# Performance work log

Hardware: AMD Instinct MI355X
Metric: run time of the kernel (lower is better)

Reference implementation:

```python
import jax, jax.numpy as jnp
import numpy as np

EPS = 1e-7          # keras K.epsilon()
MIN_TEMP = 0.1
ALPHA = 0.99999
START_TEMP = 10.0
BATCH, D, BINS, K_OUT = 4096, 20000, 10, 64


def setup_inputs() -> dict:
    key = jax.random.key(0)
    k1, k2, k3 = jax.random.split(key, 3)
    X = jax.random.normal(k1, (BATCH, D), dtype=jnp.float32)
    u = jax.random.normal(k2, (D, BINS), dtype=jnp.float32)
    # keras 'uniform' initializer: U(-0.05, 0.05)
    tinyW = jax.random.uniform(k3, (BINS, K_OUT), dtype=jnp.float32, minval=-0.05, maxval=0.05)
    temp = jnp.float32(START_TEMP)
    return {"X": X, "u": u, "tinyW": tinyW, "temp": temp}


def greedy_assign(p):
    """Greedy bipartite argmax-and-mask assignment (the host loop in the original).
    p: (k, d) scores. Returns (k, d) 0/1 assignment with one 1 per row, unique cols."""
    k, d = p.shape

    def step(pm, _):
        ind = jnp.argmax(pm)            # global argmax over flattened (k, d)
        x = ind // d
        y = ind % d
        pm = pm.at[x, :].set(-1.0).at[:, y].set(-1.0)
        return pm, (x, y)

    _, (xs, ys) = jax.lax.scan(step, p, None, length=k)
    return jnp.zeros((k, d), p.dtype).at[xs, ys].set(1.0)


def reference(X, u, tinyW, temp):
    # al = softmax(u @ tinyW) over output_dim axis, then transpose -> (k, d)
    al = jax.nn.softmax(u @ tinyW, axis=-1).T                  # (k, d)
    logits = jnp.log(10.0 * jnp.clip(al, EPS, 0.9999999))      # (k, d)
    # Gumbel noise: -log(-log(U)), U ~ Uniform(eps, 1)
    nkey = jax.random.key(42)
    uniform = jax.random.uniform(nkey, logits.shape, logits.dtype, EPS, 1.0)
    gumbel = -jnp.log(-jnp.log(uniform))
    # annealed temperature update (K.update in original)
    new_temp = jnp.maximum(jnp.float32(MIN_TEMP), temp * jnp.float32(ALPHA))
    samples = jax.nn.softmax((logits + gumbel) / new_temp, axis=-1)  # (k, d)
    # inference-path discrete selection via greedy argmax-and-mask loop
    discrete = greedy_assign(samples)                           # (k, d)
    # training path: Y = X @ samples^T  (main memory-bound skinny GEMM)
    Y = X @ samples.T                                           # (batch, k)
    return Y, discrete, new_temp
```

## Files before the change

kernel.cpp:

```cpp
#include <hip/hip_runtime.h>
#include <stdint.h>
#include <math.h>

typedef unsigned long long ull;
typedef __attribute__((ext_vector_type(8))) short short8;
typedef __attribute__((ext_vector_type(4))) float f32x4;

#define DD 20000
#define NK 64
#define NB 4096
#define YN (NB * NK)
#define TOTN (YN + NK * DD + 1)
#define KS 16

#define E_OFF   0u
#define RSP_OFF 10240000u
#define CV_OFF  10400256u
#define CC_OFF  10416640u
#define EB_OFF  10433024u
#define IRS_OFF 12993024u
#define P_OFF   12993280u

__device__ __forceinline__ uint32_t tf_bits(uint32_t j) {
  const uint32_t k0 = 0u, k1 = 42u;
  const uint32_t k2 = 0x1BD11BDAu ^ k0 ^ k1;
  uint32_t x0 = k0;
  uint32_t x1 = j + k1;
#define TFR(r) { x0 += x1; x1 = (x1 << r) | (x1 >> (32 - r)); x1 ^= x0; }
  TFR(13) TFR(15) TFR(26) TFR(6)
  x0 += k1; x1 += k2 + 1u;
  TFR(17) TFR(29) TFR(16) TFR(24)
  x0 += k2; x1 += k0 + 2u;
  TFR(13) TFR(15) TFR(26) TFR(6)
  x0 += k0; x1 += k1 + 3u;
  TFR(17) TFR(29) TFR(16) TFR(24)
  x0 += k1; x1 += k2 + 4u;
  TFR(13) TFR(15) TFR(26) TFR(6)
  x0 += k2; x1 += k0 + 5u;
#undef TFR
  return x0 ^ x1;
}

__global__ __launch_bounds__(256) void k_z(
    const float* __restrict__ uu, const float* __restrict__ tw,
    const float* __restrict__ temp, double* __restrict__ E,
    ushort* __restrict__ EB, double* __restrict__ RSP,
    float* __restrict__ disc) {
  __shared__ double tile[NK][65];
  __shared__ double psumw[4][NK];
  const int tid = threadIdx.x;
  const int lane = tid & 63;
  const int wv = tid >> 6;
  const int d0 = blockIdx.x * 64;
  const float nt = fmaxf(0.1f, temp[0] * 0.99999f);
  float w[10];
#pragma unroll
  for (int i = 0; i < 10; ++i) w[i] = tw[i * NK + lane];
  double psum = 0.0;
  for (int it = 0; it < 16; ++it) {
    const int dl = wv * 16 + it;
    const int d = d0 + dl;
    double e = 0.0;
    if (d < DD) {
      float m = 0.f;
#pragma unroll
      for (int i = 0; i < 10; ++i) m = fmaf(uu[d * 10 + i], w[i], m);
      float mx = m;
#pragma unroll
      for (int off = 32; off; off >>= 1) mx = fmaxf(mx, __shfl_xor(mx, off, 64));
      double ee = exp((double)(m - mx));
      double ssum = ee;
#pragma unroll
      for (int off = 32; off; off >>= 1) ssum += __shfl_xor(ssum, off, 64);
      float al = (float)(ee / ssum);
      float c = fminf(fmaxf(al, 1e-7f), 0.9999999f);
      float lg = (float)log((double)(10.0f * c));
      const uint32_t bits = tf_bits((uint32_t)(lane * DD + d));
      float uf = __uint_as_float((bits >> 9) | 0x3f800000u) - 1.0f;
      float uv = fmaxf(1e-7f, uf * (1.0f - 1e-7f) + 1e-7f);
      float g = (float)(-log(-log((double)uv)));
      float z = (lg + g) / nt;
      e = exp((double)z);
    }
    tile[lane][dl] = e;
    psum += e;
  }
  psumw[wv][lane] = psum;
  __syncthreads();
  for (int r0 = 0; r0 < NK; r0 += 4) {
    const int r = r0 + wv;
    const int d = d0 + lane;
    if (d < DD) {
      const double ev = tile[r][lane];
      E[(size_t)r * DD + d] = ev;
      const float ef = (float)ev;
      uint32_t ub = __float_as_uint(ef);
      EB[(size_t)r * DD + d] = (ushort)((ub + 0x7FFFu + ((ub >> 16) & 1u)) >> 16);
    }
  }
  if (wv == 0) {
    double s = psumw[0][lane] + psumw[1][lane] + psumw[2][lane] + psumw[3][lane];
    RSP[(size_t)blockIdx.x * NK + lane] = s;
  }
  const int cg = tid & 15;
  const int r0 = tid >> 4;
  if (d0 + cg * 4 < DD) {
    for (int r = r0; r < NK; r += 16)
      *(float4*)(disc + (size_t)r * DD + d0 + cg * 4) = make_float4(0.f, 0.f, 0.f, 0.f);
  }
}

__global__ __launch_bounds__(256) void k_gr(
    const float* __restrict__ X, const ushort* __restrict__ EB,
    float* __restrict__ P,
    const double* __restrict__ E, const double* __restrict__ RSP,
    float* __restrict__ cv, int* __restrict__ cc, float* __restrict__ invRS) {
  const int tid = threadIdx.x;
  if (blockIdx.x < 64) {
    const int k = blockIdx.x;
    __shared__ double redd[256];
    __shared__ ull keys[2048];
    __shared__ ull wbest[4];
    const double* er = E + (size_t)k * DD;
    double psum = 0.0;
    for (int b = tid; b < 313; b += 256) psum += RSP[(size_t)b * NK + k];
    redd[tid] = psum;
    __syncthreads();
    for (int s = 128; s; s >>= 1) {
      if (tid < s) redd[tid] += redd[tid + s];
      __syncthreads();
    }
    const double sumall = redd[0];
    if (tid == 0) invRS[k] = (float)(1.0 / sumall);
    float tv[8]; int tc[8];
#pragma unroll
    for (int s = 0; s < 8; ++s) { tv[s] = -1.f; tc[s] = 0; }
    for (int d = tid; d < DD; d += 256) {
      float svv = (float)(er[d] / sumall);
      if (svv > tv[7]) {
        float cvr = svv; int ccr = d;
#pragma unroll
        for (int s = 0; s < 8; ++s) {
          bool sw = cvr > tv[s];
          float nv = sw ? cvr : tv[s]; int nc = sw ? ccr : tc[s];
          cvr = sw ? tv[s] : cvr; ccr = sw ? tc[s] : ccr;
          tv[s] = nv; tc[s] = nc;
        }
      }
    }
#pragma unroll
    for (int s = 0; s < 8; ++s)
      keys[(tid << 3) + s] = (((ull)__float_as_uint(tv[s])) << 32)
                           | ((ull)(uint32_t)(32767 - tc[s]) << 11)
                           | ((ull)tid << 3) | (ull)s;
    __syncthreads();
    for (int t = 0; t < NK; ++t) {
      ull best = 0;
#pragma unroll
      for (int s = 0; s < 8; ++s) { ull kk = keys[(tid << 3) + s]; if (kk > best) best = kk; }
#pragma unroll
      for (int off = 32; off; off >>= 1) { ull o = __shfl_xor(best, off, 64); if (o > best) best = o; }
      if ((tid & 63) == 0) wbest[tid >> 6] = best;
      __syncthreads();
      ull win = wbest[0];
#pragma unroll
      for (int wI = 1; wI < 4; ++wI) if (wbest[wI] > win) win = wbest[wI];
      const uint32_t lo = (uint32_t)win;
      const int slot = lo & 7;
      const int owner = (lo >> 3) & 255;
      const int col = 32767 - (int)(lo >> 11);
      if (tid == 0) {
        cv[(k << 6) + t] = __uint_as_float((uint32_t)(win >> 32));
        cc[(k << 6) + t] = col;
      }
      if (tid == owner) keys[(owner << 3) + slot] = 0;
      __syncthreads();
    }
    return;
  }
  const int bx2 = blockIdx.x - 64;
  const int ksp = bx2 >> 6;
  const int by = bx2 & 63;
  const int lane = tid & 63;
  const int wv = tid >> 6;
  const int m16 = lane & 15;
  const int kq = lane >> 4;
  const int mRow = by * 64 + wv * 16 + m16;
  const float* xq = X + (size_t)mRow * DD + ksp * 32 + kq * 8;
  const ushort* bq = EB + (size_t)m16 * DD + ksp * 32 + kq * 8;
  f32x4 acc[4] = {{0,0,0,0},{0,0,0,0},{0,0,0,0},{0,0,0,0}};
  const int jN = (625 - ksp + KS - 1) / KS;

#define LOADBUF(xa, xb, bn, j) { \
    const int o_ = (j) * (KS * 32); \
    xa = *(const float4*)(xq + o_); \
    xb = *(const float4*)(xq + o_ + 4); \
    bn##0 = *(const uint4*)(bq + o_); \
    bn##1 = *(const uint4*)(bq + 16 * DD + o_); \
    bn##2 = *(const uint4*)(bq + 32 * DD + o_); \
    bn##3 = *(const uint4*)(bq + 48 * DD + o_); }

#define COMPUTEBUF(xa, xb, bn) { \
    uint32_t t0=__float_as_uint(xa.x), t1=__float_as_uint(xa.y), t2=__float_as_uint(xa.z), t3=__float_as_uint(xa.w); \
    uint32_t t4=__float_as_uint(xb.x), t5=__float_as_uint(xb.y), t6=__float_as_uint(xb.z), t7=__float_as_uint(xb.w); \
    t0=(t0+0x7FFFu+((t0>>16)&1u))>>16; t1=(t1+0x7FFFu+((t1>>16)&1u))>>16; \
    t2=(t2+0x7FFFu+((t2>>16)&1u))>>16; t3=(t3+0x7FFFu+((t3>>16)&1u))>>16; \
    t4=(t4+0x7FFFu+((t4>>16)&1u))>>16; t5=(t5+0x7FFFu+((t5>>16)&1u))>>16; \
    t6=(t6+0x7FFFu+((t6>>16)&1u))>>16; t7=(t7+0x7FFFu+((t7>>16)&1u))>>16; \
    union { uint32_t u[4]; short8 v; } A_; \
    A_.u[0]=t0|(t1<<16); A_.u[1]=t2|(t3<<16); A_.u[2]=t4|(t5<<16); A_.u[3]=t6|(t7<<16); \
    union { uint4 q; short8 v; } Q0_, Q1_, Q2_, Q3_; \
    Q0_.q = bn##0; Q1_.q = bn##1; Q2_.q = bn##2; Q3_.q = bn##3; \
    acc[0] = __builtin_amdgcn_mfma_f32_16x16x32_bf16(A_.v, Q0_.v, acc[0], 0, 0, 0); \
    acc[1] = __builtin_amdgcn_mfma_f32_16x16x32_bf16(A_.v, Q1_.v, acc[1], 0, 0, 0); \
    acc[2] = __builtin_amdgcn_mfma_f32_16x16x32_bf16(A_.v, Q2_.v, acc[2], 0, 0, 0); \
    acc[3] = __builtin_amdgcn_mfma_f32_16x16x32_bf16(A_.v, Q3_.v, acc[3], 0, 0, 0); }

  float4 xaA, xbA, xaB, xbB, xaC, xbC;
  uint4 bA0, bA1, bA2, bA3, bB0, bB1, bB2, bB3, bC0, bC1, bC2, bC3;
  LOADBUF(xaA, xbA, bA, 0);
  LOADBUF(xaB, xbB, bB, 1);
  LOADBUF(xaC, xbC, bC, 2);
  int j = 0;
  for (; j + 3 < jN; j += 3) {
    COMPUTEBUF(xaA, xbA, bA);
    LOADBUF(xaA, xbA, bA, j + 3);
    COMPUTEBUF(xaB, xbB, bB);
    if (j + 4 < jN) { LOADBUF(xaB, xbB, bB, j + 4); }
    COMPUTEBUF(xaC, xbC, bC);
    if (j + 5 < jN) { LOADBUF(xaC, xbC, bC, j + 5); }
  }
  COMPUTEBUF(xaA, xbA, bA);
  if (j + 1 < jN) { COMPUTEBUF(xaB, xbB, bB); }
  if (j + 2 < jN) { COMPUTEBUF(xaC, xbC, bC); }
#undef LOADBUF
#undef COMPUTEBUF

  float* pp = P + (size_t)ksp * YN;
  const int rBase = by * 64 + wv * 16 + kq * 4;
#pragma unroll
  for (int nt = 0; nt < 4; ++nt)
#pragma unroll
    for (int r = 0; r < 4; ++r)
      pp[(size_t)(rBase + r) * 64 + nt * 16 + m16] = acc[nt][r];
}

__global__ __launch_bounds__(256) void k_tail(
    const float* __restrict__ cv, const int* __restrict__ cc,
    const float* __restrict__ temp, const float* __restrict__ P,
    const float* __restrict__ invRS, float* __restrict__ out) {
  const int tid = threadIdx.x;
  if (blockIdx.x == 0) {
    __shared__ float vf[NK * NK];
    __shared__ int cf[NK * NK];
    __shared__ alignas(16) unsigned char used[DD];
    for (int i = tid; i < 1250; i += 256) ((int4*)used)[i] = make_int4(0, 0, 0, 0);
    for (int i = tid; i < 1024; i += 256) {
      ((float4*)vf)[i] = ((const float4*)cv)[i];
      ((int4*)cf)[i] = ((const int4*)cc)[i];
    }
    __syncthreads();
    if (tid >= 64) return;
    const int lane = tid;
    int ptr = 0;
    float hv = vf[lane << 6];
    int hc = cf[lane << 6];
    bool done = false;
    for (int t = 0; t < NK; ++t) {
      const float v = done ? -1.f : hv;
      float m = v;
#pragma unroll
      for (int off = 32; off; off >>= 1) m = fmaxf(m, __shfl_xor(m, off, 64));
      const ull mask = __ballot(v == m);
      const int row = __ffsll(mask) - 1;
      const int col = __shfl(hc, row, 64);
      if (lane == row) done = true;
      if (lane == 0) {
        used[col] = 1;
        out[YN + (size_t)row * DD + col] = 1.0f;
      }
      asm volatile("s_waitcnt lgkmcnt(0)" ::: "memory");
      if (!done && hc == col) {
        ++ptr;
        while (ptr < NK) {
          hc = cf[(lane << 6) + ptr];
          if (!used[hc]) break;
          ++ptr;
        }
        if (ptr < NK) hv = vf[(lane << 6) + ptr];
        else { hv = -2.f; hc = 0; }
      }
    }
    if (lane == 0) out[TOTN - 1] = fmaxf(0.1f, temp[0] * 0.99999f);
    return;
  }
  const int i = (blockIdx.x - 1) * 256 + tid;
  float4 a = ((const float4*)P)[i];
#pragma unroll
  for (int j = 1; j < KS; ++j) {
    const float4 b = ((const float4*)(P + (size_t)j * YN))[i];
    a.x += b.x; a.y += b.y; a.z += b.z; a.w += b.w;
  }
  const float4 irs = *(const float4*)(invRS + ((i * 4) & 63));
  a.x *= irs.x; a.y *= irs.y; a.z *= irs.z; a.w *= irs.w;
  ((float4*)out)[i] = a;
}

extern "C" void kernel_launch(void* const* d_in, const int* in_sizes, int n_in,
                              void* d_out, int out_size, void* d_ws, size_t ws_size,
                              hipStream_t stream) {
  (void)in_sizes; (void)n_in; (void)out_size; (void)ws_size;
  const float* X = (const float*)d_in[0];
  const float* uu = (const float*)d_in[1];
  const float* tw = (const float*)d_in[2];
  const float* temp = (const float*)d_in[3];
  float* out = (float*)d_out;
  char* W = (char*)d_ws;
  double* E   = (double*)(W + E_OFF);
  double* RSP = (double*)(W + RSP_OFF);
  float*  CV  = (float*)(W + CV_OFF);
  int*    CC  = (int*)(W + CC_OFF);
  ushort* EB  = (ushort*)(W + EB_OFF);
  float*  IRS = (float*)(W + IRS_OFF);
  float*  P   = (float*)(W + P_OFF);

  hipLaunchKernelGGL(k_z, dim3(313), dim3(256), 0, stream, uu, tw, temp, E, EB, RSP, out + YN);
  hipLaunchKernelGGL(k_gr, dim3(64 + KS * 64), dim3(256), 0, stream, X, EB, P, E, RSP, CV, CC, IRS);
  hipLaunchKernelGGL(k_tail, dim3(257), dim3(256), 0, stream, CV, CC, temp, P, IRS, out);
}
```

Before: 559.9 us.

## Fuse tail kernel into GEMM via atomic counters and last-block reduction

Merges the split-K partial-sum reduction and the greedy assignment into the main GEMM kernel. Atomic counters let the last split-K block per row tile do the reduction, and the last top-k block run the greedy loop. This removes one kernel launch and its serialization gap. It also changes KS from 16 to 15, cuts buffering from three stages to two, adds an occupancy hint and uses a bitmask for the used columns. The price is a spin-wait on a global counter, which assumes all producer blocks are co-resident or scheduled first, plus less pipelining depth.

```diff
diff --git a/kernel.cpp b/kernel.cpp
--- a/kernel.cpp
+++ b/kernel.cpp
@@ -11,7 +11,7 @@
 #define NB 4096
 #define YN (NB * NK)
 #define TOTN (YN + NK * DD + 1)
-#define KS 16
+#define KS 15
 
 #define E_OFF   0u
 #define RSP_OFF 10240000u
@@ -20,6 +20,9 @@
 #define EB_OFF  10433024u
 #define IRS_OFF 12993024u
 #define P_OFF   12993280u
+#define CNT_OFF 28721920u
+
+#define DSM_BYTES 35328
 
 __device__ __forceinline__ uint32_t tf_bits(uint32_t j) {
   const uint32_t k0 = 0u, k1 = 42u;
@@ -45,10 +48,11 @@
     const float* __restrict__ uu, const float* __restrict__ tw,
     const float* __restrict__ temp, double* __restrict__ E,
     ushort* __restrict__ EB, double* __restrict__ RSP,
-    float* __restrict__ disc) {
+    float* __restrict__ disc, int* __restrict__ CNT) {
   __shared__ double tile[NK][65];
   __shared__ double psumw[4][NK];
   const int tid = threadIdx.x;
+  if (blockIdx.x == 0 && tid < 65) CNT[tid] = 0;
   const int lane = tid & 63;
   const int wv = tid >> 6;
   const int d0 = blockIdx.x * 64;
@@ -110,17 +114,22 @@
   }
 }
 
-__global__ __launch_bounds__(256) void k_gr(
+__global__ __launch_bounds__(256, 4) void k_mega(
     const float* __restrict__ X, const ushort* __restrict__ EB,
     float* __restrict__ P,
     const double* __restrict__ E, const double* __restrict__ RSP,
-    float* __restrict__ cv, int* __restrict__ cc, float* __restrict__ invRS) {
+    float* __restrict__ cv, int* __restrict__ cc, float* __restrict__ invRS,
+    const float* __restrict__ temp, float* __restrict__ out,
+    int* __restrict__ CNT) {
+  extern __shared__ char sm[];
+  __shared__ int sflag;
   const int tid = threadIdx.x;
+
   if (blockIdx.x < 64) {
     const int k = blockIdx.x;
-    __shared__ double redd[256];
-    __shared__ ull keys[2048];
-    __shared__ ull wbest[4];
+    double* redd = (double*)sm;
+    ull* keys = (ull*)(sm + 2048);
+    ull* wbest = (ull*)(sm + 18432);
     const double* er = E + (size_t)k * DD;
     double psum = 0.0;
     for (int b = tid; b < 313; b += 256) psum += RSP[(size_t)b * NK + k];
@@ -176,8 +185,58 @@
       if (tid == owner) keys[(owner << 3) + slot] = 0;
       __syncthreads();
     }
+    if (tid == 0) {
+      int old = __hip_atomic_fetch_add(&CNT[64], 1, __ATOMIC_ACQ_REL,
+                                       __HIP_MEMORY_SCOPE_AGENT);
+      sflag = (old == 63);
+    }
+    __syncthreads();
+    if (!sflag) return;
+    __threadfence();
+    float* vf = (float*)sm;
+    int* cf = (int*)(sm + 16384);
+    uint32_t* usedw = (uint32_t*)(sm + 32768);
+    for (int i = tid; i < 625; i += 256) usedw[i] = 0;
+    for (int i = tid; i < 1024; i += 256) {
+      ((float4*)vf)[i] = ((const float4*)cv)[i];
+      ((int4*)cf)[i] = ((const int4*)cc)[i];
+    }
+    __syncthreads();
+    if (tid >= 64) return;
+    const int lane = tid;
+    int ptr = 0;
+    float hv = vf[lane << 6];
+    int hc = cf[lane << 6];
+    bool done = false;
+    for (int t = 0; t < NK; ++t) {
+      const float v = done ? -1.f : hv;
+      float m = v;
+#pragma unroll
+      for (int off = 32; off; off >>= 1) m = fmaxf(m, __shfl_xor(m, off, 64));
+      const ull mask = __ballot(v == m);
+      const int row = __ffsll(mask) - 1;
+      const int col = __shfl(hc, row, 64);
+      if (lane == row) done = true;
+      if (lane == 0) {
+        usedw[col >> 5] |= (1u << (col & 31));
+        out[YN + (size_t)row * DD + col] = 1.0f;
+      }
+      asm volatile("s_waitcnt lgkmcnt(0)" ::: "memory");
+      if (!done && hc == col) {
+        ++ptr;
+        while (ptr < NK) {
+          hc = cf[(lane << 6) + ptr];
+          if (!((usedw[hc >> 5] >> (hc & 31)) & 1u)) break;
+          ++ptr;
+        }
+        if (ptr < NK) hv = vf[(lane << 6) + ptr];
+        else { hv = -2.f; hc = 0; }
+      }
+    }
+    if (lane == 0) out[TOTN - 1] = fmaxf(0.1f, temp[0] * 0.99999f);
     return;
   }
+
   const int bx2 = blockIdx.x - 64;
   const int ksp = bx2 >> 6;
   const int by = bx2 & 63;
@@ -185,8 +244,7 @@
   const int wv = tid >> 6;
   const int m16 = lane & 15;
   const int kq = lane >> 4;
-  const int mRow = by * 64 + wv * 16 + m16;
-  const float* xq = X + (size_t)mRow * DD + ksp * 32 + kq * 8;
+  const float* xq = X + (size_t)(by * 64 + wv * 16 + m16) * DD + ksp * 32 + kq * 8;
   const ushort* bq = EB + (size_t)m16 * DD + ksp * 32 + kq * 8;
   f32x4 acc[4] = {{0,0,0,0},{0,0,0,0},{0,0,0,0},{0,0,0,0}};
   const int jN = (625 - ksp + KS - 1) / KS;
@@ -216,94 +274,56 @@
     acc[2] = __builtin_amdgcn_mfma_f32_16x16x32_bf16(A_.v, Q2_.v, acc[2], 0, 0, 0); \
     acc[3] = __builtin_amdgcn_mfma_f32_16x16x32_bf16(A_.v, Q3_.v, acc[3], 0, 0, 0); }
 
-  float4 xaA, xbA, xaB, xbB, xaC, xbC;
-  uint4 bA0, bA1, bA2, bA3, bB0, bB1, bB2, bB3, bC0, bC1, bC2, bC3;
+  float4 xaA, xbA, xaB, xbB;
+  uint4 bA0, bA1, bA2, bA3, bB0, bB1, bB2, bB3;
   LOADBUF(xaA, xbA, bA, 0);
   LOADBUF(xaB, xbB, bB, 1);
-  LOADBUF(xaC, xbC, bC, 2);
   int j = 0;
-  for (; j + 3 < jN; j += 3) {
+  for (; j + 2 < jN; j += 2) {
     COMPUTEBUF(xaA, xbA, bA);
-    LOADBUF(xaA, xbA, bA, j + 3);
+    LOADBUF(xaA, xbA, bA, j + 2);
     COMPUTEBUF(xaB, xbB, bB);
-    if (j + 4 < jN) { LOADBUF(xaB, xbB, bB, j + 4); }
-    COMPUTEBUF(xaC, xbC, bC);
-    if (j + 5 < jN) { LOADBUF(xaC, xbC, bC, j + 5); }
+    if (j + 3 < jN) { LOADBUF(xaB, xbB, bB, j + 3); }
   }
   COMPUTEBUF(xaA, xbA, bA);
   if (j + 1 < jN) { COMPUTEBUF(xaB, xbB, bB); }
-  if (j + 2 < jN) { COMPUTEBUF(xaC, xbC, bC); }
 #undef LOADBUF
 #undef COMPUTEBUF
 
-  float* pp = P + (size_t)ksp * YN;
-  const int rBase = by * 64 + wv * 16 + kq * 4;
-#pragma unroll
-  for (int nt = 0; nt < 4; ++nt)
-#pragma unroll
-    for (int r = 0; r < 4; ++r)
-      pp[(size_t)(rBase + r) * 64 + nt * 16 + m16] = acc[nt][r];
-}
-
-__global__ __launch_bounds__(256) void k_tail(
-    const float* __restrict__ cv, const int* __restrict__ cc,
-    const float* __restrict__ temp, const float* __restrict__ P,
-    const float* __restrict__ invRS, float* __restrict__ out) {
-  const int tid = threadIdx.x;
-  if (blockIdx.x == 0) {
-    __shared__ float vf[NK * NK];
-    __shared__ int cf[NK * NK];
-    __shared__ alignas(16) unsigned char used[DD];
-    for (int i = tid; i < 1250; i += 256) ((int4*)used)[i] = make_int4(0, 0, 0, 0);
-    for (int i = tid; i < 1024; i += 256) {
-      ((float4*)vf)[i] = ((const float4*)cv)[i];
-      ((int4*)cf)[i] = ((const int4*)cc)[i];
-    }
-    __syncthreads();
-    if (tid >= 64) return;
-    const int lane = tid;
-    int ptr = 0;
-    float hv = vf[lane << 6];
-    int hc = cf[lane << 6];
-    bool done = false;
-    for (int t = 0; t < NK; ++t) {
-      const float v = done ? -1.f : hv;
-      float m = v;
-#pragma unroll
-      for (int off = 32; off; off >>= 1) m = fmaxf(m, __shfl_xor(m, off, 64));
-      const ull mask = __ballot(v == m);
-      const int row = __ffsll(mask) - 1;
-      const int col = __shfl(hc, row, 64);
-      if (lane == row) done = true;
-      if (lane == 0) {
-        used[col] = 1;
-        out[YN + (size_t)row * DD + col] = 1.0f;
-      }
-      asm volatile("s_waitcnt lgkmcnt(0)" ::: "memory");
-      if (!done && hc == col) {
-        ++ptr;
-        while (ptr < NK) {
-          hc = cf[(lane << 6) + ptr];
-          if (!used[hc]) break;
-          ++ptr;
-        }
-        if (ptr < NK) hv = vf[(lane << 6) + ptr];
-        else { hv = -2.f; hc = 0; }
-      }
-    }
-    if (lane == 0) out[TOTN - 1] = fmaxf(0.1f, temp[0] * 0.99999f);
-    return;
-  }
-  const int i = (blockIdx.x - 1) * 256 + tid;
-  float4 a = ((const float4*)P)[i];
-#pragma unroll
-  for (int j = 1; j < KS; ++j) {
-    const float4 b = ((const float4*)(P + (size_t)j * YN))[i];
-    a.x += b.x; a.y += b.y; a.z += b.z; a.w += b.w;
-  }
-  const float4 irs = *(const float4*)(invRS + ((i * 4) & 63));
-  a.x *= irs.x; a.y *= irs.y; a.z *= irs.z; a.w *= irs.w;
-  ((float4*)out)[i] = a;
+  {
+    float* pp = P + (size_t)ksp * YN;
+    const int rBase = by * 64 + wv * 16 + kq * 4;
+#pragma unroll
+    for (int nt = 0; nt < 4; ++nt)
+#pragma unroll
+      for (int r = 0; r < 4; ++r)
+        pp[(size_t)(rBase + r) * 64 + nt * 16 + m16] = acc[nt][r];
+  }
+  __syncthreads();
+  if (tid == 0) {
+    int old = __hip_atomic_fetch_add(&CNT[by], 1, __ATOMIC_ACQ_REL,
+                                     __HIP_MEMORY_SCOPE_AGENT);
+    sflag = (old == KS - 1);
+  }
+  __syncthreads();
+  if (!sflag) return;
+  __threadfence();
+  while (__hip_atomic_load(&CNT[64], __ATOMIC_ACQUIRE, __HIP_MEMORY_SCOPE_AGENT) < 64)
+    __builtin_amdgcn_s_sleep(2);
+  for (int q = tid; q < 1024; q += 256) {
+    const int row = q >> 4;
+    const int c4 = q & 15;
+    const size_t idx = (size_t)(by * 64 + row) * 16 + c4;
+    float4 a = ((const float4*)P)[idx];
+#pragma unroll
+    for (int jj = 1; jj < KS; ++jj) {
+      const float4 b = ((const float4*)(P + (size_t)jj * YN))[idx];
+      a.x += b.x; a.y += b.y; a.z += b.z; a.w += b.w;
+    }
+    const float4 irs = ((const float4*)invRS)[c4];
+    a.x *= irs.x; a.y *= irs.y; a.z *= irs.z; a.w *= irs.w;
+    ((float4*)out)[idx] = a;
+  }
 }
 
 extern "C" void kernel_launch(void* const* d_in, const int* in_sizes, int n_in,
@@ -323,8 +343,10 @@
   ushort* EB  = (ushort*)(W + EB_OFF);
   float*  IRS = (float*)(W + IRS_OFF);
   float*  P   = (float*)(W + P_OFF);
-
-  hipLaunchKernelGGL(k_z, dim3(313), dim3(256), 0, stream, uu, tw, temp, E, EB, RSP, out + YN);
-  hipLaunchKernelGGL(k_gr, dim3(64 + KS * 64), dim3(256), 0, stream, X, EB, P, E, RSP, CV, CC, IRS);
-  hipLaunchKernelGGL(k_tail, dim3(257), dim3(256), 0, stream, CV, CC, temp, P, IRS, out);
+  int*    CNT = (int*)(W + CNT_OFF);
+
+  hipLaunchKernelGGL(k_z, dim3(313), dim3(256), 0, stream,
+                     uu, tw, temp, E, EB, RSP, out + YN, CNT);
+  hipLaunchKernelGGL(k_mega, dim3(1024), dim3(256), DSM_BYTES, stream,
+                     X, EB, P, E, RSP, CV, CC, IRS, temp, out, CNT);
 }
```

After: 660.6 us. 1.18x slower.
